# Kernel tuning notes

Measured on AMD Instinct MI355X. Metric: run time of the kernel, lower is better.

## Reference

```python
import jax, jax.numpy as jnp
import numpy as np

B, T, N_EMBD, HEAD_SIZE = 64, 512, 384, 64


def setup_inputs() -> dict:
    key = jax.random.key(0)
    k1, k2, k3, k4 = jax.random.split(key, 4)
    x = jax.random.normal(k1, (B, T, N_EMBD), dtype=jnp.float32)
    scale = 1.0 / np.sqrt(N_EMBD)
    Wq = jax.random.normal(k2, (N_EMBD, HEAD_SIZE), dtype=jnp.float32) * scale
    Wk = jax.random.normal(k3, (N_EMBD, HEAD_SIZE), dtype=jnp.float32) * scale
    Wv = jax.random.normal(k4, (N_EMBD, HEAD_SIZE), dtype=jnp.float32) * scale
    return {"x": x, "Wq": Wq, "Wk": Wk, "Wv": Wv}


def reference(x, Wq, Wk, Wv):
    # Single-head causal self-attention (dropout = identity / eval mode).
    q = jnp.einsum('btc,ch->bth', x, Wq)  # [B,T,H]
    k = jnp.einsum('btc,ch->bth', x, Wk)
    v = jnp.einsum('btc,ch->bth', x, Wv)
    scale = q.shape[-1] ** -0.5
    scores = jnp.einsum('bth,bsh->bts', q, k) * scale  # [B,T,T]
    Tlen = x.shape[1]
    causal = jnp.tril(jnp.ones((Tlen, Tlen), dtype=bool))
    scores = jnp.where(causal, scores, -jnp.inf)
    weights = jax.nn.softmax(scores, axis=-1)
    out = jnp.einsum('bts,bsh->bth', weights, v)  # [B,T,H]
    return out
```

## Files before the change

### kernel.cpp

```cpp
#include <hip/hip_runtime.h>


typedef __bf16 bf16_t;
typedef __bf16 bf16x8 __attribute__((ext_vector_type(8)));
typedef __bf16 bf16x4 __attribute__((ext_vector_type(4)));
typedef float  f32x4  __attribute__((ext_vector_type(4)));

__device__ __forceinline__ bf16x8 ld_b128(const bf16_t* p) {
    return *reinterpret_cast<const bf16x8*>(p);
}

__global__ __launch_bounds__(256) void wt_kernel(const float* __restrict__ Wq,
                                                 const float* __restrict__ Wk,
                                                 const float* __restrict__ Wv,
                                                 bf16_t* __restrict__ Wt) {
    int idx = blockIdx.x * 256 + threadIdx.x;
    int p = idx / (384 * 64);
    int r = idx - p * (384 * 64);
    int c = r >> 6;
    int h = r & 63;
    const float* W = (p == 0) ? Wq : (p == 1) ? Wk : Wv;
    Wt[p * 24576 + h * 384 + c] = (bf16_t)W[c * 64 + h];
}

__global__ __launch_bounds__(256, 2) void qkv_kernel(const float* __restrict__ x,
                                                     const bf16_t* __restrict__ Wt,
                                                     bf16_t* __restrict__ Q,
                                                     bf16_t* __restrict__ K,
                                                     bf16_t* __restrict__ Vt) {
    const int tid  = threadIdx.x;
    const int wave = tid >> 6, lane = tid & 63;
    const int quad = lane >> 4, l16 = lane & 15;
    const int rowbase = blockIdx.x * 64;
    const int batch   = rowbase >> 9;

    __shared__ alignas(16) bf16_t xs[64][392];

    bf16x8 Bf[3][12];
    #pragma unroll
    for (int nt = 0; nt < 3; ++nt) {
        int col  = wave * 48 + nt * 16 + l16;
        int proj = col >> 6, h = col & 63;
        const bf16_t* wp = Wt + proj * 24576 + h * 384 + quad * 8;
        #pragma unroll
        for (int kk = 0; kk < 12; ++kk) Bf[nt][kk] = ld_b128(wp + kk * 32);
    }

    #pragma unroll
    for (int i = 0; i < 12; ++i) {
        int idx = i * 256 + tid;
        int row = idx / 48;
        int p   = idx - row * 48;
        const float* src = x + (rowbase + row) * 384 + p * 8;
        float4 a = *reinterpret_cast<const float4*>(src);
        float4 c = *reinterpret_cast<const float4*>(src + 4);
        bf16x8 v = {(bf16_t)a.x, (bf16_t)a.y, (bf16_t)a.z, (bf16_t)a.w,
                    (bf16_t)c.x, (bf16_t)c.y, (bf16_t)c.z, (bf16_t)c.w};
        *reinterpret_cast<bf16x8*>(&xs[row][p * 8]) = v;
    }
    __syncthreads();

    #pragma unroll
    for (int rt = 0; rt < 4; ++rt) {
        f32x4 acc[3];
        #pragma unroll
        for (int nt = 0; nt < 3; ++nt) acc[nt] = (f32x4){0.f, 0.f, 0.f, 0.f};

        #pragma unroll
        for (int kk = 0; kk < 12; ++kk) {
            bf16x8 a = *reinterpret_cast<const bf16x8*>(&xs[rt * 16 + l16][kk * 32 + quad * 8]);
            #pragma unroll
            for (int nt = 0; nt < 3; ++nt)
                acc[nt] = __builtin_amdgcn_mfma_f32_16x16x32_bf16(a, Bf[nt][kk], acc[nt], 0, 0, 0);
        }

        #pragma unroll
        for (int nt = 0; nt < 3; ++nt) {
            int col  = wave * 48 + nt * 16 + l16;
            int proj = col >> 6, h = col & 63;
            int trow = rowbase + rt * 16 + quad * 4;
            if (proj == 0) {
                #pragma unroll
                for (int r = 0; r < 4; ++r) Q[(trow + r) * 64 + h] = (bf16_t)acc[nt][r];
            } else if (proj == 1) {
                #pragma unroll
                for (int r = 0; r < 4; ++r) K[(trow + r) * 64 + h] = (bf16_t)acc[nt][r];
            } else {
                bf16x4 v = {(bf16_t)acc[nt][0], (bf16_t)acc[nt][1],
                            (bf16_t)acc[nt][2], (bf16_t)acc[nt][3]};
                *reinterpret_cast<bf16x4*>(Vt + batch * 32768 + h * 512 + (trow & 511)) = v;
            }
        }
    }
}

__global__ __launch_bounds__(256, 2) void attn_kernel(const bf16_t* __restrict__ Q,
                                                      const bf16_t* __restrict__ K,
                                                      const bf16_t* __restrict__ Vt,
                                                      float* __restrict__ out) {
    const int tid  = threadIdx.x;
    const int wave = tid >> 6, lane = tid & 63;
    const int quad = lane >> 4, l16 = lane & 15;
    const int b    = blockIdx.x >> 3;
    const int j    = blockIdx.x & 7;
    const int ti   = j + wave * 8;
    const int rbase = ti * 16;

    __shared__ alignas(16) bf16_t Pl[4][2][16 * 64];

    const bf16_t* Kb = K  + b * 512 * 64;
    const bf16_t* Vb = Vt + b * 32768;

    const bf16_t* qptr = Q + (b * 512 + rbase + l16) * 64 + quad * 8;
    bf16x8 aq0 = ld_b128(qptr);
    bf16x8 aq1 = ld_b128(qptr + 32);

    f32x4 acc_o[4];
    #pragma unroll
    for (int nt = 0; nt < 4; ++nt) acc_o[nt] = (f32x4){0.f, 0.f, 0.f, 0.f};
    float l_lane[4] = {0.f, 0.f, 0.f, 0.f};
    const int rowq = rbase + quad * 4;

    bf16x8 KloA[4], KhiA[4], VloA[4], VhiA[4];
    bf16x8 KloB[4], KhiB[4], VloB[4], VhiB[4];

    auto loadKV = [&](bf16x8* Klo, bf16x8* Khi, bf16x8* Vlo, bf16x8* Vhi, int kb) {
        #pragma unroll
        for (int nt = 0; nt < 4; ++nt) {
            const bf16_t* kp = Kb + (kb + nt * 16 + l16) * 64 + quad * 8;
            Klo[nt] = ld_b128(kp);
            Khi[nt] = ld_b128(kp + 32);
        }
        #pragma unroll
        for (int nth = 0; nth < 4; ++nth) {
            const bf16_t* vp = Vb + (nth * 16 + l16) * 512 + kb + quad * 8;
            Vlo[nth] = ld_b128(vp);
            Vhi[nth] = ld_b128(vp + 32);
        }
    };

    auto step = [&](bf16x8* Klo, bf16x8* Khi, bf16x8* Vlo, bf16x8* Vhi,
                    int kb, bool last, int pbuf) {
        float s[4][4];
        #pragma unroll
        for (int nt = 0; nt < 4; ++nt) {
            f32x4 c = (f32x4){0.f, 0.f, 0.f, 0.f};
            c = __builtin_amdgcn_mfma_f32_16x16x32_bf16(aq0, Klo[nt], c, 0, 0, 0);
            c = __builtin_amdgcn_mfma_f32_16x16x32_bf16(aq1, Khi[nt], c, 0, 0, 0);
            #pragma unroll
            for (int r = 0; r < 4; ++r) s[nt][r] = c[r];
        }
        if (last) {
            #pragma unroll
            for (int nt = 0; nt < 4; ++nt)
                #pragma unroll
                for (int r = 0; r < 4; ++r)
                    if (kb + nt * 16 + l16 > rowq + r) s[nt][r] = -__builtin_inff();
        }
        bf16_t* pw = &Pl[wave][pbuf][0];
        #pragma unroll
        for (int nt = 0; nt < 4; ++nt) {
            #pragma unroll
            for (int r = 0; r < 4; ++r) {
                float p = __expf(fmaf(s[nt][r], 0.125f, -20.0f));
                l_lane[r] += p;
                int rl  = quad * 4 + r;
                int col = nt * 16 + l16;
                pw[rl * 64 + (((col >> 3) ^ (rl & 7)) << 3) + (col & 7)] = (bf16_t)p;
            }
        }
        bf16x8 ap0 = ld_b128(&pw[l16 * 64 + (((0 + quad) ^ (l16 & 7)) << 3)]);
        bf16x8 ap1 = ld_b128(&pw[l16 * 64 + (((4 + quad) ^ (l16 & 7)) << 3)]);
        #pragma unroll
        for (int nth = 0; nth < 4; ++nth) {
            acc_o[nth] = __builtin_amdgcn_mfma_f32_16x16x32_bf16(ap0, Vlo[nth], acc_o[nth], 0, 0, 0);
            acc_o[nth] = __builtin_amdgcn_mfma_f32_16x16x32_bf16(ap1, Vhi[nth], acc_o[nth], 0, 0, 0);
        }
    };

    const int nsteps = (rbase >> 6) + 1;
    loadKV(KloA, KhiA, VloA, VhiA, 0);
    int ks = 0;
    while (true) {
        if (ks + 1 < nsteps) loadKV(KloB, KhiB, VloB, VhiB, (ks + 1) * 64);
        step(KloA, KhiA, VloA, VhiA, ks * 64, ks == nsteps - 1, ks & 1);
        if (++ks == nsteps) break;
        if (ks + 1 < nsteps) loadKV(KloA, KhiA, VloA, VhiA, (ks + 1) * 64);
        step(KloB, KhiB, VloB, VhiB, ks * 64, ks == nsteps - 1, ks & 1);
        if (++ks == nsteps) break;
    }

    #pragma unroll
    for (int r = 0; r < 4; ++r) {
        float l = l_lane[r];
        #pragma unroll
        for (int xm = 1; xm < 16; xm <<= 1) l += __shfl_xor(l, xm, 64);
        l_lane[r] = l;
    }

    #pragma unroll
    for (int nth = 0; nth < 4; ++nth) {
        #pragma unroll
        for (int r = 0; r < 4; ++r) {
            out[(b * 512 + rowq + r) * 64 + nth * 16 + l16] =
                acc_o[nth][r] / l_lane[r];
        }
    }
}

extern "C" void kernel_launch(void* const* d_in, const int* in_sizes, int n_in,
                              void* d_out, int out_size, void* d_ws, size_t ws_size,
                              hipStream_t stream) {
    const float* x  = (const float*)d_in[0];
    const float* Wq = (const float*)d_in[1];
    const float* Wk = (const float*)d_in[2];
    const float* Wv = (const float*)d_in[3];

    char* ws = (char*)d_ws;
    bf16_t* Wt = (bf16_t*)(ws);
    bf16_t* Q  = (bf16_t*)(ws + 147456);
    bf16_t* K  = (bf16_t*)(ws + 147456 + 4194304);
    bf16_t* Vt = (bf16_t*)(ws + 147456 + 8388608);

    wt_kernel<<<dim3(288), dim3(256), 0, stream>>>(Wq, Wk, Wv, Wt);
    qkv_kernel<<<dim3(512), dim3(256), 0, stream>>>(x, Wt, Q, K, Vt);
    attn_kernel<<<dim3(512), dim3(256), 0, stream>>>(Q, K, Vt, (float*)d_out);
}
```

Baseline: 120.3 us.

## Split attention KV range across wave pairs and shrink QKV projection tiles

The attention kernel now gives each 16-row query tile to two waves, which take alternating 64-key blocks and merge partial outputs and row sums through shared memory. This halves the serial causal chain per wave and doubles the grid. The explicit register double-buffering of K/V is removed in favour of a plain loop. The QKV projection now uses 32-row blocks with 4 waves covering a 16x96 output tile each, streaming weight fragments from global memory instead of keeping them all in registers. Occupancy hints rise to 4 blocks per CU. The trade is an extra sync and LDS reduction, less load prefetch, and more re-reading of the weights.

New measurement: 151.9 us. 26.3% more time.

```diff
diff --git a/kernel.cpp b/kernel.cpp
--- a/kernel.cpp
+++ b/kernel.cpp
@@ -23,7 +23,7 @@
     Wt[p * 24576 + h * 384 + c] = (bf16_t)W[c * 64 + h];
 }
 
-__global__ __launch_bounds__(256, 2) void qkv_kernel(const float* __restrict__ x,
+__global__ __launch_bounds__(256, 4) void qkv_kernel(const float* __restrict__ x,
                                                      const bf16_t* __restrict__ Wt,
                                                      bf16_t* __restrict__ Q,
                                                      bf16_t* __restrict__ K,
@@ -31,23 +31,15 @@
     const int tid  = threadIdx.x;
     const int wave = tid >> 6, lane = tid & 63;
     const int quad = lane >> 4, l16 = lane & 15;
-    const int rowbase = blockIdx.x * 64;
+    const int rowbase = blockIdx.x * 32;
     const int batch   = rowbase >> 9;
-
-    __shared__ alignas(16) bf16_t xs[64][392];
-
-    bf16x8 Bf[3][12];
-    #pragma unroll
-    for (int nt = 0; nt < 3; ++nt) {
-        int col  = wave * 48 + nt * 16 + l16;
-        int proj = col >> 6, h = col & 63;
-        const bf16_t* wp = Wt + proj * 24576 + h * 384 + quad * 8;
-        #pragma unroll
-        for (int kk = 0; kk < 12; ++kk) Bf[nt][kk] = ld_b128(wp + kk * 32);
-    }
-
-    #pragma unroll
-    for (int i = 0; i < 12; ++i) {
+    const int wrow = (wave >> 1) * 16;
+    const int c0   = (wave & 1) * 96;
+
+    __shared__ alignas(16) bf16_t xs[32][392];
+
+    #pragma unroll
+    for (int i = 0; i < 6; ++i) {
         int idx = i * 256 + tid;
         int row = idx / 48;
         int p   = idx - row * 48;
@@ -60,53 +52,70 @@
     }
     __syncthreads();
 
-    #pragma unroll
-    for (int rt = 0; rt < 4; ++rt) {
-        f32x4 acc[3];
-        #pragma unroll
-        for (int nt = 0; nt < 3; ++nt) acc[nt] = (f32x4){0.f, 0.f, 0.f, 0.f};
-
-        #pragma unroll
-        for (int kk = 0; kk < 12; ++kk) {
-            bf16x8 a = *reinterpret_cast<const bf16x8*>(&xs[rt * 16 + l16][kk * 32 + quad * 8]);
-            #pragma unroll
-            for (int nt = 0; nt < 3; ++nt)
-                acc[nt] = __builtin_amdgcn_mfma_f32_16x16x32_bf16(a, Bf[nt][kk], acc[nt], 0, 0, 0);
-        }
-
-        #pragma unroll
-        for (int nt = 0; nt < 3; ++nt) {
-            int col  = wave * 48 + nt * 16 + l16;
-            int proj = col >> 6, h = col & 63;
-            int trow = rowbase + rt * 16 + quad * 4;
-            if (proj == 0) {
-                #pragma unroll
-                for (int r = 0; r < 4; ++r) Q[(trow + r) * 64 + h] = (bf16_t)acc[nt][r];
-            } else if (proj == 1) {
-                #pragma unroll
-                for (int r = 0; r < 4; ++r) K[(trow + r) * 64 + h] = (bf16_t)acc[nt][r];
-            } else {
-                bf16x4 v = {(bf16_t)acc[nt][0], (bf16_t)acc[nt][1],
-                            (bf16_t)acc[nt][2], (bf16_t)acc[nt][3]};
-                *reinterpret_cast<bf16x4*>(Vt + batch * 32768 + h * 512 + (trow & 511)) = v;
-            }
-        }
-    }
-}
-
-__global__ __launch_bounds__(256, 2) void attn_kernel(const bf16_t* __restrict__ Q,
+    bf16x8 A[12];
+    #pragma unroll
+    for (int kk = 0; kk < 12; ++kk)
+        A[kk] = *reinterpret_cast<const bf16x8*>(&xs[wrow + l16][kk * 32 + quad * 8]);
+
+    const bf16_t* bp[6];
+    #pragma unroll
+    for (int nt = 0; nt < 6; ++nt) {
+        int col  = c0 + nt * 16 + l16;
+        int proj = col >> 6, h = col & 63;
+        bp[nt] = Wt + proj * 24576 + h * 384 + quad * 8;
+    }
+
+    f32x4 acc[6];
+    #pragma unroll
+    for (int nt = 0; nt < 6; ++nt) acc[nt] = (f32x4){0.f, 0.f, 0.f, 0.f};
+
+    bf16x8 Bb[4];
+    #pragma unroll
+    for (int j0 = 0; j0 < 4; ++j0) Bb[j0] = ld_b128(bp[j0 % 6] + (j0 / 6) * 32);
+    #pragma unroll
+    for (int j = 0; j < 72; ++j) {
+        int kk = j / 6, nt = j % 6;
+        bf16x8 b = Bb[j & 3];
+        if (j + 4 < 72) Bb[j & 3] = ld_b128(bp[(j + 4) % 6] + ((j + 4) / 6) * 32);
+        acc[nt] = __builtin_amdgcn_mfma_f32_16x16x32_bf16(A[kk], b, acc[nt], 0, 0, 0);
+    }
+
+    #pragma unroll
+    for (int nt = 0; nt < 6; ++nt) {
+        int col  = c0 + nt * 16 + l16;
+        int proj = col >> 6, h = col & 63;
+        int trow = rowbase + wrow + quad * 4;
+        if (proj == 0) {
+            #pragma unroll
+            for (int r = 0; r < 4; ++r) Q[(trow + r) * 64 + h] = (bf16_t)acc[nt][r];
+        } else if (proj == 1) {
+            #pragma unroll
+            for (int r = 0; r < 4; ++r) K[(trow + r) * 64 + h] = (bf16_t)acc[nt][r];
+        } else {
+            bf16x4 v = {(bf16_t)acc[nt][0], (bf16_t)acc[nt][1],
+                        (bf16_t)acc[nt][2], (bf16_t)acc[nt][3]};
+            *reinterpret_cast<bf16x4*>(Vt + batch * 32768 + h * 512 + (trow & 511)) = v;
+        }
+    }
+}
+
+__global__ __launch_bounds__(256, 4) void attn_kernel(const bf16_t* __restrict__ Q,
                                                       const bf16_t* __restrict__ K,
                                                       const bf16_t* __restrict__ Vt,
                                                       float* __restrict__ out) {
     const int tid  = threadIdx.x;
     const int wave = tid >> 6, lane = tid & 63;
     const int quad = lane >> 4, l16 = lane & 15;
-    const int b    = blockIdx.x >> 3;
-    const int j    = blockIdx.x & 7;
-    const int ti   = j + wave * 8;
+    const int b    = blockIdx.x >> 4;
+    const int pair = blockIdx.x & 15;
+    const int ti   = pair * 2 + (wave >> 1);
+    const int split = wave & 1;
     const int rbase = ti * 16;
+    const int rowq  = rbase + quad * 4;
+    const int n     = (rbase >> 6) + 1;
 
     __shared__ alignas(16) bf16_t Pl[4][2][16 * 64];
+    __shared__ float Cd[2][64][21];
 
     const bf16_t* Kb = K  + b * 512 * 64;
     const bf16_t* Vb = Vt + b * 32768;
@@ -119,12 +128,12 @@
     #pragma unroll
     for (int nt = 0; nt < 4; ++nt) acc_o[nt] = (f32x4){0.f, 0.f, 0.f, 0.f};
     float l_lane[4] = {0.f, 0.f, 0.f, 0.f};
-    const int rowq = rbase + quad * 4;
-
-    bf16x8 KloA[4], KhiA[4], VloA[4], VhiA[4];
-    bf16x8 KloB[4], KhiB[4], VloB[4], VhiB[4];
-
-    auto loadKV = [&](bf16x8* Klo, bf16x8* Khi, bf16x8* Vlo, bf16x8* Vhi, int kb) {
+
+    for (int kt = split; kt < n; kt += 2) {
+        int  kb   = kt * 64;
+        bool last = (kt == n - 1);
+
+        bf16x8 Klo[4], Khi[4], Vlo[4], Vhi[4];
         #pragma unroll
         for (int nt = 0; nt < 4; ++nt) {
             const bf16_t* kp = Kb + (kb + nt * 16 + l16) * 64 + quad * 8;
@@ -137,10 +146,7 @@
             Vlo[nth] = ld_b128(vp);
             Vhi[nth] = ld_b128(vp + 32);
         }
-    };
-
-    auto step = [&](bf16x8* Klo, bf16x8* Khi, bf16x8* Vlo, bf16x8* Vhi,
-                    int kb, bool last, int pbuf) {
+
         float s[4][4];
         #pragma unroll
         for (int nt = 0; nt < 4; ++nt) {
@@ -157,7 +163,8 @@
                 for (int r = 0; r < 4; ++r)
                     if (kb + nt * 16 + l16 > rowq + r) s[nt][r] = -__builtin_inff();
         }
-        bf16_t* pw = &Pl[wave][pbuf][0];
+
+        bf16_t* pw = &Pl[wave][(kt >> 1) & 1][0];
         #pragma unroll
         for (int nt = 0; nt < 4; ++nt) {
             #pragma unroll
@@ -176,35 +183,35 @@
             acc_o[nth] = __builtin_amdgcn_mfma_f32_16x16x32_bf16(ap0, Vlo[nth], acc_o[nth], 0, 0, 0);
             acc_o[nth] = __builtin_amdgcn_mfma_f32_16x16x32_bf16(ap1, Vhi[nth], acc_o[nth], 0, 0, 0);
         }
-    };
-
-    const int nsteps = (rbase >> 6) + 1;
-    loadKV(KloA, KhiA, VloA, VhiA, 0);
-    int ks = 0;
-    while (true) {
-        if (ks + 1 < nsteps) loadKV(KloB, KhiB, VloB, VhiB, (ks + 1) * 64);
-        step(KloA, KhiA, VloA, VhiA, ks * 64, ks == nsteps - 1, ks & 1);
-        if (++ks == nsteps) break;
-        if (ks + 1 < nsteps) loadKV(KloA, KhiA, VloA, VhiA, (ks + 1) * 64);
-        step(KloB, KhiB, VloB, VhiB, ks * 64, ks == nsteps - 1, ks & 1);
-        if (++ks == nsteps) break;
-    }
-
-    #pragma unroll
-    for (int r = 0; r < 4; ++r) {
-        float l = l_lane[r];
-        #pragma unroll
-        for (int xm = 1; xm < 16; xm <<= 1) l += __shfl_xor(l, xm, 64);
-        l_lane[r] = l;
-    }
-
-    #pragma unroll
-    for (int nth = 0; nth < 4; ++nth) {
+    }
+
+    if (!(wave & 1)) {
+        #pragma unroll
+        for (int nt = 0; nt < 4; ++nt)
+            #pragma unroll
+            for (int r = 0; r < 4; ++r) Cd[wave >> 1][lane][nt * 4 + r] = acc_o[nt][r];
+        #pragma unroll
+        for (int r = 0; r < 4; ++r) Cd[wave >> 1][lane][16 + r] = l_lane[r];
+    }
+    __syncthreads();
+    if (wave & 1) {
+        #pragma unroll
+        for (int nt = 0; nt < 4; ++nt)
+            #pragma unroll
+            for (int r = 0; r < 4; ++r) acc_o[nt][r] += Cd[wave >> 1][lane][nt * 4 + r];
         #pragma unroll
         for (int r = 0; r < 4; ++r) {
-            out[(b * 512 + rowq + r) * 64 + nth * 16 + l16] =
-                acc_o[nth][r] / l_lane[r];
-        }
+            float l = l_lane[r] + Cd[wave >> 1][lane][16 + r];
+            #pragma unroll
+            for (int xm = 1; xm < 16; xm <<= 1) l += __shfl_xor(l, xm, 64);
+            l_lane[r] = l;
+        }
+        #pragma unroll
+        for (int nth = 0; nth < 4; ++nth)
+            #pragma unroll
+            for (int r = 0; r < 4; ++r)
+                out[(b * 512 + rowq + r) * 64 + nth * 16 + l16] =
+                    acc_o[nth][r] / l_lane[r];
     }
 }
 
@@ -223,6 +230,6 @@
     bf16_t* Vt = (bf16_t*)(ws + 147456 + 8388608);
 
     wt_kernel<<<dim3(288), dim3(256), 0, stream>>>(Wq, Wk, Wv, Wt);
-    qkv_kernel<<<dim3(512), dim3(256), 0, stream>>>(x, Wt, Q, K, Vt);
-    attn_kernel<<<dim3(512), dim3(256), 0, stream>>>(Q, K, Vt, (float*)d_out);
-}
+    qkv_kernel<<<dim3(1024), dim3(256), 0, stream>>>(x, Wt, Q, K, Vt);
+    attn_kernel<<<dim3(1024), dim3(256), 0, stream>>>(Q, K, Vt, (float*)d_out);
+}
```

## Stage shared K/V tiles in LDS via async global-to-LDS copies

Applied to the files above, without the earlier changes.

Each attention block now handles one contiguous 64-row query tile, split across its four waves. The block stages each 64-key K and V^T tile once into swizzled, double-buffered LDS using global_load_lds 16-byte copies. Previously every wave loaded its own K/V fragments from global memory into registers, so this cuts redundant L2/global traffic and register pressure. The cost is an extra block-wide barrier per step, and load imbalance across blocks, since causal work now grows with the tile index rather than being interleaved across waves.

Result: faster. 115.0 us (-4.4%).

```diff
diff --git a/kernel.cpp b/kernel.cpp
--- a/kernel.cpp
+++ b/kernel.cpp
@@ -8,6 +8,13 @@
 
 __device__ __forceinline__ bf16x8 ld_b128(const bf16_t* p) {
     return *reinterpret_cast<const bf16x8*>(p);
+}
+
+__device__ __forceinline__ void async_copy16(void* lds, const void* g) {
+    __builtin_amdgcn_global_load_lds(
+        (const __attribute__((address_space(1))) unsigned int*)g,
+        (__attribute__((address_space(3))) unsigned int*)lds,
+        16, 0, 0);
 }
 
 __global__ __launch_bounds__(256) void wt_kernel(const float* __restrict__ Wq,
@@ -103,12 +110,14 @@
     const int quad = lane >> 4, l16 = lane & 15;
     const int b    = blockIdx.x >> 3;
     const int j    = blockIdx.x & 7;
-    const int ti   = j + wave * 8;
-    const int rbase = ti * 16;
-
-    __shared__ alignas(16) bf16_t Pl[4][2][16 * 64];
-
-    const bf16_t* Kb = K  + b * 512 * 64;
+    const int rbase = j * 64 + wave * 16;
+    const int rowq  = rbase + quad * 4;
+
+    __shared__ alignas(16) bf16_t Kt[2][64 * 64];
+    __shared__ alignas(16) bf16_t Vtt[2][64 * 64];
+    __shared__ alignas(16) bf16_t Pl[4][16 * 64];
+
+    const bf16_t* Kb = K  + b * 32768;
     const bf16_t* Vb = Vt + b * 32768;
 
     const bf16_t* qptr = Q + (b * 512 + rbase + l16) * 64 + quad * 8;
@@ -119,34 +128,36 @@
     #pragma unroll
     for (int nt = 0; nt < 4; ++nt) acc_o[nt] = (f32x4){0.f, 0.f, 0.f, 0.f};
     float l_lane[4] = {0.f, 0.f, 0.f, 0.f};
-    const int rowq = rbase + quad * 4;
-
-    bf16x8 KloA[4], KhiA[4], VloA[4], VhiA[4];
-    bf16x8 KloB[4], KhiB[4], VloB[4], VhiB[4];
-
-    auto loadKV = [&](bf16x8* Klo, bf16x8* Khi, bf16x8* Vlo, bf16x8* Vhi, int kb) {
+
+    auto stage = [&](int buf, int kb) {
+        #pragma unroll
+        for (int i = 0; i < 2; ++i) {
+            int rr = wave * 16 + i * 8 + (lane >> 3);
+            int g  = (lane & 7) ^ (rr & 7);
+            async_copy16(&Kt[buf][(wave * 16 + i * 8) * 64],
+                         Kb + (kb + rr) * 64 + g * 8);
+            async_copy16(&Vtt[buf][(wave * 16 + i * 8) * 64],
+                         Vb + rr * 512 + kb + g * 8);
+        }
+    };
+
+    stage(0, 0);
+    for (int kt = 0; kt <= j; ++kt) {
+        int buf = kt & 1;
+        __syncthreads();
+        if (kt < j) stage(1 - buf, (kt + 1) * 64);
+        int kb = kt * 64;
+        bool last = (kt == j);
+
+        float s[4][4];
         #pragma unroll
         for (int nt = 0; nt < 4; ++nt) {
-            const bf16_t* kp = Kb + (kb + nt * 16 + l16) * 64 + quad * 8;
-            Klo[nt] = ld_b128(kp);
-            Khi[nt] = ld_b128(kp + 32);
-        }
-        #pragma unroll
-        for (int nth = 0; nth < 4; ++nth) {
-            const bf16_t* vp = Vb + (nth * 16 + l16) * 512 + kb + quad * 8;
-            Vlo[nth] = ld_b128(vp);
-            Vhi[nth] = ld_b128(vp + 32);
-        }
-    };
-
-    auto step = [&](bf16x8* Klo, bf16x8* Khi, bf16x8* Vlo, bf16x8* Vhi,
-                    int kb, bool last, int pbuf) {
-        float s[4][4];
-        #pragma unroll
-        for (int nt = 0; nt < 4; ++nt) {
+            int tk = nt * 16 + l16;
             f32x4 c = (f32x4){0.f, 0.f, 0.f, 0.f};
-            c = __builtin_amdgcn_mfma_f32_16x16x32_bf16(aq0, Klo[nt], c, 0, 0, 0);
-            c = __builtin_amdgcn_mfma_f32_16x16x32_bf16(aq1, Khi[nt], c, 0, 0, 0);
+            bf16x8 bk0 = ld_b128(&Kt[buf][tk * 64 + (((0 + quad) ^ (tk & 7)) << 3)]);
+            c = __builtin_amdgcn_mfma_f32_16x16x32_bf16(aq0, bk0, c, 0, 0, 0);
+            bf16x8 bk1 = ld_b128(&Kt[buf][tk * 64 + (((4 + quad) ^ (tk & 7)) << 3)]);
+            c = __builtin_amdgcn_mfma_f32_16x16x32_bf16(aq1, bk1, c, 0, 0, 0);
             #pragma unroll
             for (int r = 0; r < 4; ++r) s[nt][r] = c[r];
         }
@@ -157,7 +168,8 @@
                 for (int r = 0; r < 4; ++r)
                     if (kb + nt * 16 + l16 > rowq + r) s[nt][r] = -__builtin_inff();
         }
-        bf16_t* pw = &Pl[wave][pbuf][0];
+
+        bf16_t* pw = &Pl[wave][0];
         #pragma unroll
         for (int nt = 0; nt < 4; ++nt) {
             #pragma unroll
@@ -173,21 +185,12 @@
         bf16x8 ap1 = ld_b128(&pw[l16 * 64 + (((4 + quad) ^ (l16 & 7)) << 3)]);
         #pragma unroll
         for (int nth = 0; nth < 4; ++nth) {
-            acc_o[nth] = __builtin_amdgcn_mfma_f32_16x16x32_bf16(ap0, Vlo[nth], acc_o[nth], 0, 0, 0);
-            acc_o[nth] = __builtin_amdgcn_mfma_f32_16x16x32_bf16(ap1, Vhi[nth], acc_o[nth], 0, 0, 0);
-        }
-    };
-
-    const int nsteps = (rbase >> 6) + 1;
-    loadKV(KloA, KhiA, VloA, VhiA, 0);
-    int ks = 0;
-    while (true) {
-        if (ks + 1 < nsteps) loadKV(KloB, KhiB, VloB, VhiB, (ks + 1) * 64);
-        step(KloA, KhiA, VloA, VhiA, ks * 64, ks == nsteps - 1, ks & 1);
-        if (++ks == nsteps) break;
-        if (ks + 1 < nsteps) loadKV(KloA, KhiA, VloA, VhiA, (ks + 1) * 64);
-        step(KloB, KhiB, VloB, VhiB, ks * 64, ks == nsteps - 1, ks & 1);
-        if (++ks == nsteps) break;
+            int h = nth * 16 + l16;
+            bf16x8 bv0 = ld_b128(&Vtt[buf][h * 64 + (((0 + quad) ^ (h & 7)) << 3)]);
+            acc_o[nth] = __builtin_amdgcn_mfma_f32_16x16x32_bf16(ap0, bv0, acc_o[nth], 0, 0, 0);
+            bf16x8 bv1 = ld_b128(&Vtt[buf][h * 64 + (((4 + quad) ^ (h & 7)) << 3)]);
+            acc_o[nth] = __builtin_amdgcn_mfma_f32_16x16x32_bf16(ap1, bv1, acc_o[nth], 0, 0, 0);
+        }
     }
 
     #pragma unroll
```
